# Optimization experiments

Measured on AMD Instinct MI355X. Metric: run time of the kernel, lower is better.

The kernel has to match this reference:

```python
import jax, jax.numpy as jnp
import numpy as np

B, N, C, H, NC, P = 16, 577, 768, 12, 8, 576  # batch, seq(=patches+cls), dim, heads, curves, patches
D = C // H


def setup_inputs() -> dict:
    key = jax.random.key(0)
    ks = jax.random.split(key, 8)
    x = jax.random.normal(ks[0], (B, N, C), jnp.float32)
    qkv_w = jax.random.normal(ks[1], (C, 3 * C), jnp.float32) * 0.02
    proj_w = jax.random.normal(ks[2], (C, C), jnp.float32) * 0.02
    proj_b = jnp.zeros((C,), jnp.float32)
    # learned per-head decay logits; +3 so sigmoid ~0.95 (slow decay, realistic)
    ai_list = jax.random.normal(ks[3], (NC, H), jnp.float32) + 3.0
    mask_weights = jax.random.normal(ks[4], (NC,), jnp.float32) * 0.1 + 1.0 / NC
    normalize = 1.0 + 0.1 * jax.random.normal(ks[5], (H,), jnp.float32)
    # space-filling-curve inverse index permutations (one per curve)
    curve_inds = jnp.stack([
        jax.random.permutation(jax.random.fold_in(ks[6], c), P) for c in range(NC)
    ]).astype(jnp.int32)
    return dict(x=x, qkv_w=qkv_w, proj_w=proj_w, proj_b=proj_b,
                ai_list=ai_list, mask_weights=mask_weights,
                normalize=normalize, curve_inds=curve_inds)


def _build_mask(ai_list, mask_weights, curve_inds):
    # sigmoid(a)^|i-j| gathered by the curve permutation == sigmoid(a)^|ind_i - ind_j|
    a = jax.nn.sigmoid(ai_list)                                  # [NC,H]
    ci = curve_inds.astype(jnp.float32)                          # [NC,P]
    diff = jnp.abs(ci[:, :, None] - ci[:, None, :])              # [NC,P,P]
    Mc = a[:, :, None, None] ** diff[:, None, :, :]              # [NC,H,P,P]
    Mp = jnp.einsum('c,chpq->hpq', mask_weights, Mc)             # weighted sum over curves
    # cls-token row/col: each curve contributes ones -> sum of weights
    sw = jnp.sum(mask_weights)
    M = jnp.pad(Mp, ((0, 0), (1, 0), (1, 0)))                    # [H,N,N]
    M = M.at[:, 0, :].set(sw)
    M = M.at[:, :, 0].set(sw)
    return M


def reference(x, qkv_w, proj_w, proj_b, ai_list, mask_weights, normalize, curve_inds):
    qkv = (x @ qkv_w).reshape(B, N, 3, H, D)
    q = jnp.transpose(qkv[:, :, 0], (0, 2, 1, 3))                # [B,H,N,D]
    k = jnp.transpose(qkv[:, :, 1], (0, 2, 1, 3))
    v = jnp.transpose(qkv[:, :, 2], (0, 2, 1, 3))
    # NOTE: original overwrites self.scale with the bool `scale`=True -> multiply by 1
    attn = jnp.einsum('bhnd,bhmd->bhnm', q, k)                   # [B,H,N,N]
    M = _build_mask(ai_list, mask_weights, curve_inds)           # [H,N,N]
    attn = attn * M[None] * normalize[None, :, None, None]       # method='mul_v1'
    attn = jax.nn.softmax(attn, axis=-1)
    out = jnp.einsum('bhnm,bhmd->bhnd', attn, v)
    out = jnp.transpose(out, (0, 2, 1, 3)).reshape(B, N, C)
    return out @ proj_w + proj_b
```

## Files before the change

kernel.cpp:

```cpp
#include <hip/hip_runtime.h>


typedef _Float16 f16;
typedef _Float16 half8 __attribute__((ext_vector_type(8)));
typedef _Float16 half4 __attribute__((ext_vector_type(4)));
typedef float floatx4 __attribute__((ext_vector_type(4)));

#define DEVINL __device__ __forceinline__

#define Bb 16
#define NN 577
#define CC 768
#define HH 12
#define DD 64
#define MM (Bb * NN)
#define VTLD 584
#define MLD 580
#define CLD 136

DEVINL void async_copy16(void* lds, const void* g) {
  __builtin_amdgcn_global_load_lds(
      (const __attribute__((address_space(1))) void*)g,
      (__attribute__((address_space(3))) void*)lds, 16, 0, 0);
}

DEVINL half8 ld_swz(const f16* lds, int row, int chunk) {
  return *(const half8*)(lds + row * 64 + ((chunk ^ (row & 7)) << 3));
}

DEVINL int xcd_swizzle(int orig, int nwg) {
  int q = nwg >> 3, r = nwg & 7;
  int xcd = orig & 7, loc = orig >> 3;
  return (xcd < r ? xcd * (q + 1) : r * (q + 1) + (xcd - r) * q) + loc;
}

__global__ void cvt_kernel(const float* __restrict__ in, f16* __restrict__ out, int n) {
  int i = (blockIdx.x * blockDim.x + threadIdx.x) * 4;
  if (i >= n) return;
  float4 v = *(const float4*)(in + i);
  half4 o = {(f16)v.x, (f16)v.y, (f16)v.z, (f16)v.w};
  *(half4*)(out + i) = o;
}

__global__ void transpose_cvt(const float* __restrict__ in, f16* __restrict__ out,
                              int N3, int K) {
  __shared__ float t[32][33];
  const int k0 = blockIdx.x * 32, n0 = blockIdx.y * 32;
  const int tx = threadIdx.x & 31, ty = threadIdx.x >> 5;
#pragma unroll
  for (int p = 0; p < 4; ++p)
    t[ty + p * 8][tx] = in[(size_t)(k0 + ty + p * 8) * N3 + n0 + tx];
  __syncthreads();
#pragma unroll
  for (int p = 0; p < 4; ++p)
    out[(size_t)(n0 + ty + p * 8) * K + k0 + tx] = (f16)t[tx][ty + p * 8];
}

__global__ void mask_kernel(const float* __restrict__ ai, const float* __restrict__ mw,
                            const float* __restrict__ nrm, const int* __restrict__ ci,
                            float* __restrict__ Mb) {
  const int i = blockIdx.x;
  const int h = blockIdx.y;
  __shared__ float la_s[8], wv_s[8], cif[8], swn_s;
  int tid = threadIdx.x;
  if (tid < 8) {
    float av = ai[tid * 12 + h];
    float a = 1.f / (1.f + __expf(-av));
    la_s[tid] = __logf(a);
    wv_s[tid] = mw[tid];
    cif[tid] = (i > 0) ? (float)ci[tid * 576 + (i - 1)] : 0.f;
  }
  if (tid == 0) {
    float s = 0.f;
    for (int c = 0; c < 8; ++c) s += mw[c];
    swn_s = s * nrm[h] * 1.44269504088896f;
  }
  __syncthreads();
  const float nr = nrm[h] * 1.44269504088896f;
  float* row = Mb + ((size_t)h * NN + i) * MLD;
  for (int j = tid; j < NN; j += blockDim.x) {
    float val;
    if (i == 0 || j == 0) {
      val = swn_s;
    } else {
      float acc = 0.f;
#pragma unroll
      for (int c = 0; c < 8; ++c) {
        float d = fabsf(cif[c] - (float)ci[c * 576 + (j - 1)]);
        acc += wv_s[c] * __expf(la_s[c] * d);
      }
      val = acc * nr;
    }
    row[j] = val;
  }
}

DEVINL void gemm_mainloop(const f16* __restrict__ A, const f16* __restrict__ Bt,
                          int arow0, int brow0, int maxar,
                          f16* SMEM, floatx4 acc[4][4], int tid) {
  const int lane = tid & 63;
  const int wid = tid >> 6;
  const int wr = wid >> 1, wc = wid & 1;
  const int l15 = lane & 15, g = lane >> 4;
  const int r_ = tid >> 3, cp_ = tid & 7;
  const int lc_ = (cp_ ^ (r_ & 7)) << 3;

  auto stage = [&](f16* As, f16* Bs, int k0) {
#pragma unroll
    for (int q = 0; q < 4; ++q) {
      int idx = q * 256 + tid;
      int r = q * 32 + r_;
      int ar = arow0 + r; if (ar > maxar) ar = maxar;
      async_copy16(As + idx * 8, A + (size_t)ar * CC + k0 + lc_);
      async_copy16(Bs + idx * 8, Bt + (size_t)(brow0 + r) * CC + k0 + lc_);
    }
  };
  auto compute = [&](const f16* As, const f16* Bs) {
#pragma unroll
    for (int kk = 0; kk < 2; ++kk) {
      half8 af[4], bf[4];
#pragma unroll
      for (int mi = 0; mi < 4; ++mi) af[mi] = ld_swz(As, wr * 64 + mi * 16 + l15, kk * 4 + g);
#pragma unroll
      for (int ni = 0; ni < 4; ++ni) bf[ni] = ld_swz(Bs, wc * 64 + ni * 16 + l15, kk * 4 + g);
#pragma unroll
      for (int mi = 0; mi < 4; ++mi)
#pragma unroll
        for (int ni = 0; ni < 4; ++ni)
          acc[mi][ni] = __builtin_amdgcn_mfma_f32_16x16x32_f16(af[mi], bf[ni], acc[mi][ni], 0, 0, 0);
    }
  };

  const int nt = CC / 64;
  stage(SMEM, SMEM + 8192, 0);
#pragma unroll 1
  for (int t = 0; t < nt; ++t) {
    f16* cAs = (t & 1) ? SMEM + 16384 : SMEM;
    f16* cBs = (t & 1) ? SMEM + 24576 : SMEM + 8192;
    f16* nAs = (t & 1) ? SMEM : SMEM + 16384;
    f16* nBs = (t & 1) ? SMEM + 8192 : SMEM + 24576;
    if (t + 1 < nt) {
      stage(nAs, nBs, (t + 1) * 64);
      asm volatile("s_waitcnt vmcnt(8)" ::: "memory");
    } else {
      asm volatile("s_waitcnt vmcnt(0)" ::: "memory");
    }
    __builtin_amdgcn_s_barrier();
    __builtin_amdgcn_sched_barrier(0);
    compute(cAs, cBs);
    __builtin_amdgcn_s_barrier();
  }
}

__global__ __launch_bounds__(256, 2)
void gemm_qkv(const f16* __restrict__ A, const f16* __restrict__ Bt,
              f16* __restrict__ qb, f16* __restrict__ kb, f16* __restrict__ vt) {
  __shared__ __align__(16) f16 SMEM[32768];
  floatx4 acc[4][4] = {};
  const int nwg = 18 * 73;
  const int wgid = xcd_swizzle(blockIdx.y * gridDim.x + blockIdx.x, nwg);
  const int m0 = (wgid / 18) * 128, n0 = (wgid % 18) * 128;
  gemm_mainloop(A, Bt, m0, n0, MM - 1, SMEM, acc, threadIdx.x);
  const int tid = threadIdx.x, lane = tid & 63, wid = tid >> 6;
  const int wr = wid >> 1, wc = wid & 1, l15 = lane & 15, g = lane >> 4;
  const int t = n0 / CC;
  const int h0 = (n0 - t * CC) >> 6;
  if (t < 2) {
#pragma unroll
    for (int mi = 0; mi < 4; ++mi)
#pragma unroll
      for (int ni = 0; ni < 4; ++ni)
#pragma unroll
        for (int r = 0; r < 4; ++r)
          SMEM[(wr * 64 + mi * 16 + 4 * g + r) * CLD + wc * 64 + ni * 16 + l15] =
              (f16)acc[mi][ni][r];
    __syncthreads();
    f16* dst = (t == 0) ? qb : kb;
#pragma unroll
    for (int p = 0; p < 8; ++p) {
      int c = p * 256 + tid;
      int ml = c >> 4, n3c = (c & 15) << 3;
      int mg = m0 + ml;
      if (mg < MM) {
        int b = mg / NN, n = mg - b * NN;
        int h = h0 + (n3c >> 6), d0 = n3c & 63;
        half8 v = *(const half8*)(SMEM + ml * CLD + n3c);
        *(half8*)(dst + ((size_t)(b * HH + h) * NN + n) * DD + d0) = v;
      }
    }
  } else {
#pragma unroll
    for (int mi = 0; mi < 4; ++mi)
#pragma unroll
      for (int ni = 0; ni < 4; ++ni)
#pragma unroll
        for (int r = 0; r < 4; ++r)
          SMEM[(wc * 64 + ni * 16 + l15) * CLD + wr * 64 + mi * 16 + 4 * g + r] =
              (f16)acc[mi][ni][r];
    __syncthreads();
#pragma unroll
    for (int p = 0; p < 8; ++p) {
      int c = p * 256 + tid;
      int n3 = c >> 4, mc = (c & 15) << 3;
      int mg = m0 + mc;
      int h = h0 + (n3 >> 6), d = n3 & 63;
      half8 v = *(const half8*)(SMEM + n3 * CLD + mc);
      int b0 = mg / NN, b7 = (mg + 7) / NN;
      if (mg + 7 < MM && b0 == b7) {
        *(half8*)(vt + ((size_t)(b0 * HH + h) * DD + d) * VTLD + (mg - b0 * NN)) = v;
      } else {
#pragma unroll
        for (int e = 0; e < 8; ++e) {
          int m2 = mg + e;
          if (m2 < MM) {
            int b = m2 / NN;
            vt[((size_t)(b * HH + h) * DD + d) * VTLD + (m2 - b * NN)] = v[e];
          }
        }
      }
    }
  }
}

__global__ __launch_bounds__(256, 2)
void gemm_proj(const f16* __restrict__ A, const f16* __restrict__ Bt,
               const float* __restrict__ bias, float* __restrict__ out) {
  __shared__ __align__(16) f16 SMEM[32768];
  floatx4 acc[4][4] = {};
  const int nwg = 6 * 73;
  const int wgid = xcd_swizzle(blockIdx.y * gridDim.x + blockIdx.x, nwg);
  const int m0 = (wgid / 6) * 128, n0 = (wgid % 6) * 128;
  gemm_mainloop(A, Bt, m0, n0, MM - 1, SMEM, acc, threadIdx.x);
  const int lane = threadIdx.x & 63, wid = threadIdx.x >> 6;
  const int wr = wid >> 1, wc = wid & 1, l15 = lane & 15, g = lane >> 4;
#pragma unroll
  for (int mi = 0; mi < 4; ++mi)
#pragma unroll
    for (int ni = 0; ni < 4; ++ni)
#pragma unroll
      for (int r = 0; r < 4; ++r) {
        int m = m0 + wr * 64 + mi * 16 + 4 * g + r;
        if (m >= MM) continue;
        int n = n0 + wc * 64 + ni * 16 + l15;
        out[(size_t)m * CC + n] = acc[mi][ni][r] + bias[n];
      }
}

__global__ __launch_bounds__(512, 4)
void attn_kernel(const f16* __restrict__ qb, const f16* __restrict__ kb,
                 const f16* __restrict__ vt, const float* __restrict__ Mb,
                 f16* __restrict__ aout) {
  __shared__ f16 Ks[2][64 * 64];
  __shared__ f16 Vs[2][64 * 64];
  const int D0 = (blockIdx.z * gridDim.y + blockIdx.y) * gridDim.x + blockIdx.x;
  const int wgid = xcd_swizzle(D0, 5 * HH * Bb);
  const int it = wgid % 5;
  const int rem = wgid / 5;
  const int b = rem % Bb, h = rem / Bb;
  const int tid = threadIdx.x, lane = tid & 63, wid = tid >> 6;
  const int l15 = lane & 15, g = lane >> 4;
  const size_t bh = (size_t)b * HH + h;
  const f16* qbh = qb + bh * NN * DD;
  const f16* kbh = kb + bh * NN * DD;
  const f16* vbh = vt + bh * DD * VTLD;
  const float* Mh = Mb + (size_t)h * NN * MLD;
  const int row0w = it * 128 + wid * 16;

  half8 qB0, qB1;
  {
    int qr = row0w + l15; if (qr > NN - 1) qr = NN - 1;
    const f16* qp = qbh + (size_t)qr * DD + g * 8;
    qB0 = *(const half8*)qp;
    qB1 = *(const half8*)(qp + 32);
  }
  const float* Mrow;
  {
    int r0 = row0w + l15; if (r0 > NN - 1) r0 = NN - 1;
    Mrow = Mh + (size_t)r0 * MLD + 4 * g;
  }

  floatx4 acc[4] = {};
  float lsum = 0.f;
  float mrun = -3e38f;

  const int sr_ = tid >> 3, scp_ = tid & 7;
  const int slc_ = (scp_ ^ (sr_ & 7)) << 3;
  auto stage = [&](f16* Kd, f16* Vd, int j0) {
    int j = j0 + sr_; if (j > NN - 1) j = NN - 1;
    async_copy16(Kd + tid * 8, kbh + (size_t)j * DD + slc_);
    async_copy16(Vd + tid * 8, vbh + (size_t)sr_ * VTLD + j0 + slc_);
  };
  auto ldmask = [&](floatx4 m4[4], int j0) {
#pragma unroll
    for (int jt = 0; jt < 4; ++jt)
      m4[jt] = *(const floatx4*)(Mrow + j0 + jt * 16);
  };
  auto compute = [&](const f16* Kc, const f16* Vc, floatx4 m4[4], int j0) {
    floatx4 sf[4];
#pragma unroll
    for (int jt = 0; jt < 4; ++jt) {
      half8 ka0 = ld_swz(Kc, jt * 16 + l15, g);
      half8 ka1 = ld_swz(Kc, jt * 16 + l15, 4 + g);
      floatx4 z = {0.f, 0.f, 0.f, 0.f};
      z = __builtin_amdgcn_mfma_f32_16x16x32_f16(ka0, qB0, z, 0, 0, 0);
      z = __builtin_amdgcn_mfma_f32_16x16x32_f16(ka1, qB1, z, 0, 0, 0);
      sf[jt] = z;
    }
#pragma unroll
    for (int jt = 0; jt < 4; ++jt)
#pragma unroll
      for (int r = 0; r < 4; ++r) sf[jt][r] *= m4[jt][r];
    if (j0 + 64 > NN) {
#pragma unroll
      for (int jt = 0; jt < 4; ++jt)
#pragma unroll
        for (int r = 0; r < 4; ++r)
          if (j0 + jt * 16 + 4 * g + r >= NN) sf[jt][r] = -3e38f;
    }
    float pj[4];
#pragma unroll
    for (int jt = 0; jt < 4; ++jt)
      pj[jt] = fmaxf(fmaxf(sf[jt][0], sf[jt][1]), fmaxf(sf[jt][2], sf[jt][3]));
    float pmax = fmaxf(fmaxf(pj[0], pj[1]), fmaxf(pj[2], pj[3]));
    pmax = fmaxf(pmax, __shfl_xor(pmax, 16));
    pmax = fmaxf(pmax, __shfl_xor(pmax, 32));
    if (!__all(pmax - mrun <= 8.f)) {
      float mnew = fmaxf(mrun, pmax);
      float fac = __builtin_amdgcn_exp2f(mrun - mnew);
      mrun = mnew;
      lsum *= fac;
#pragma unroll
      for (int dt = 0; dt < 4; ++dt)
#pragma unroll
        for (int r = 0; r < 4; ++r) acc[dt][r] *= fac;
    }
    half4 pB[4];
    float lsj[4];
#pragma unroll
    for (int jt = 0; jt < 4; ++jt) {
      half4 pb;
      float p0 = __builtin_amdgcn_exp2f(sf[jt][0] - mrun);
      float p1 = __builtin_amdgcn_exp2f(sf[jt][1] - mrun);
      float p2 = __builtin_amdgcn_exp2f(sf[jt][2] - mrun);
      float p3 = __builtin_amdgcn_exp2f(sf[jt][3] - mrun);
      pb[0] = (f16)p0; pb[1] = (f16)p1; pb[2] = (f16)p2; pb[3] = (f16)p3;
      lsj[jt] = (p0 + p1) + (p2 + p3);
      pB[jt] = pb;
    }
    lsum += (lsj[0] + lsj[1]) + (lsj[2] + lsj[3]);
#pragma unroll
    for (int dt = 0; dt < 4; ++dt)
#pragma unroll
      for (int jt = 0; jt < 4; ++jt) {
        int c16 = (jt * 2 + (g >> 1)) ^ (l15 & 7);
        half4 va = *(const half4*)(Vc + (dt * 16 + l15) * 64 + (c16 << 3) + (g & 1) * 4);
        acc[dt] = __builtin_amdgcn_mfma_f32_16x16x16f16(va, pB[jt], acc[dt], 0, 0, 0);
      }
  };

  floatx4 m4A[4], m4B[4];
  stage(Ks[0], Vs[0], 0);
  ldmask(m4A, 0);

#pragma unroll 1
  for (int t = 0; t < 10; t += 2) {
    ldmask(m4B, (t + 1) * 64);
    asm volatile("s_waitcnt vmcnt(4)" ::: "memory");
    __builtin_amdgcn_s_barrier();
    __builtin_amdgcn_sched_barrier(0);
    stage(Ks[1], Vs[1], (t + 1) * 64);
    compute(Ks[0], Vs[0], m4A, t * 64);
    const int j2 = (t + 2 < 10) ? (t + 2) * 64 : 0;
    ldmask(m4A, j2);
    asm volatile("s_waitcnt vmcnt(4)" ::: "memory");
    __builtin_amdgcn_s_barrier();
    __builtin_amdgcn_sched_barrier(0);
    stage(Ks[0], Vs[0], j2);
    compute(Ks[1], Vs[1], m4B, (t + 1) * 64);
  }

  {
    float v = lsum;
    v += __shfl_xor(v, 16);
    v += __shfl_xor(v, 32);
    float linv = 1.f / v;
    int n = row0w + l15;
    if (n < NN) {
#pragma unroll
      for (int dt = 0; dt < 4; ++dt) {
        half4 o;
#pragma unroll
        for (int r = 0; r < 4; ++r) o[r] = (f16)(acc[dt][r] * linv);
        *(half4*)(aout + ((size_t)(b * NN + n)) * CC + h * DD + dt * 16 + 4 * g) = o;
      }
    }
  }
}

extern "C" void kernel_launch(void* const* d_in, const int* in_sizes, int n_in,
                              void* d_out, int out_size, void* d_ws, size_t ws_size,
                              hipStream_t stream) {
  const float* x    = (const float*)d_in[0];
  const float* qkvw = (const float*)d_in[1];
  const float* pw   = (const float*)d_in[2];
  const float* pb   = (const float*)d_in[3];
  const float* ai   = (const float*)d_in[4];
  const float* mw   = (const float*)d_in[5];
  const float* nrm  = (const float*)d_in[6];
  const int*   ci   = (const int*)d_in[7];
  float* out = (float*)d_out;

  char* wsb = (char*)d_ws;
  size_t off = 0;
  auto alloc = [&](size_t bytes) {
    char* p = wsb + off;
    off += (bytes + 255) & ~(size_t)255;
    return p;
  };
  f16*   x_h  = (f16*)alloc((size_t)MM * CC * 2);
  f16*   w_t  = (f16*)alloc((size_t)3 * CC * CC * 2);
  f16*   pw_t = (f16*)alloc((size_t)CC * CC * 2);
  float* Mb   = (float*)alloc((size_t)HH * NN * MLD * 4 + 1024);
  f16*   qb   = (f16*)alloc((size_t)Bb * HH * NN * DD * 2);
  f16*   kb   = (f16*)alloc((size_t)Bb * HH * NN * DD * 2);
  f16*   vt   = (f16*)alloc((size_t)Bb * HH * DD * VTLD * 2);
  (void)alloc(4096);
  f16* aout = x_h;

  cvt_kernel<<<(MM * CC / 4 + 255) / 256, 256, 0, stream>>>(x, x_h, MM * CC);
  transpose_cvt<<<dim3(CC / 32, 3 * CC / 32), 256, 0, stream>>>(qkvw, w_t, 3 * CC, CC);
  transpose_cvt<<<dim3(CC / 32, CC / 32), 256, 0, stream>>>(pw, pw_t, CC, CC);
  mask_kernel<<<dim3(NN, HH), 256, 0, stream>>>(ai, mw, nrm, ci, Mb);
  gemm_qkv<<<dim3(18, 73), 256, 0, stream>>>(x_h, w_t, qb, kb, vt);
  attn_kernel<<<dim3(5, HH, Bb), 512, 0, stream>>>(qb, kb, vt, Mb, aout);
  gemm_proj<<<dim3(6, 73), 256, 0, stream>>>(aout, pw_t, pb, out);
}
```

Measured before the change: 159.4 us.

## Merge prep kernels into one launch and use 256x128 GEMM tiles with 512 threads

Folds the fp16 convert, the two weight transpose-converts and the mask build into a single prep kernel that dispatches on block index, removing three kernel launches. Both GEMMs move from 128x128 tiles with 256 threads to 256x128 tiles with 512 threads, so each staged B tile is reused by twice as many A rows. LDS grows to 96KB per block, which limits occupancy. The larger M tile also raises tail waste, since the 9232 rows now fill 37 row tiles instead of 73.

Measured after the change: 150.3 us. -5.7%, faster.

```diff
diff --git a/kernel.cpp b/kernel.cpp
--- a/kernel.cpp
+++ b/kernel.cpp
@@ -17,6 +17,7 @@
 #define VTLD 584
 #define MLD 580
 #define CLD 136
+#define TLD 264
 
 DEVINL void async_copy16(void* lds, const void* g) {
   __builtin_amdgcn_global_load_lds(
@@ -34,64 +35,71 @@
   return (xcd < r ? xcd * (q + 1) : r * (q + 1) + (xcd - r) * q) + loc;
 }
 
-__global__ void cvt_kernel(const float* __restrict__ in, f16* __restrict__ out, int n) {
-  int i = (blockIdx.x * blockDim.x + threadIdx.x) * 4;
-  if (i >= n) return;
-  float4 v = *(const float4*)(in + i);
-  half4 o = {(f16)v.x, (f16)v.y, (f16)v.z, (f16)v.w};
-  *(half4*)(out + i) = o;
-}
-
-__global__ void transpose_cvt(const float* __restrict__ in, f16* __restrict__ out,
-                              int N3, int K) {
-  __shared__ float t[32][33];
-  const int k0 = blockIdx.x * 32, n0 = blockIdx.y * 32;
-  const int tx = threadIdx.x & 31, ty = threadIdx.x >> 5;
-#pragma unroll
-  for (int p = 0; p < 4; ++p)
-    t[ty + p * 8][tx] = in[(size_t)(k0 + ty + p * 8) * N3 + n0 + tx];
-  __syncthreads();
-#pragma unroll
-  for (int p = 0; p < 4; ++p)
-    out[(size_t)(n0 + ty + p * 8) * K + k0 + tx] = (f16)t[tx][ty + p * 8];
-}
-
-__global__ void mask_kernel(const float* __restrict__ ai, const float* __restrict__ mw,
-                            const float* __restrict__ nrm, const int* __restrict__ ci,
-                            float* __restrict__ Mb) {
-  const int i = blockIdx.x;
-  const int h = blockIdx.y;
-  __shared__ float la_s[8], wv_s[8], cif[8], swn_s;
-  int tid = threadIdx.x;
-  if (tid < 8) {
-    float av = ai[tid * 12 + h];
-    float a = 1.f / (1.f + __expf(-av));
-    la_s[tid] = __logf(a);
-    wv_s[tid] = mw[tid];
-    cif[tid] = (i > 0) ? (float)ci[tid * 576 + (i - 1)] : 0.f;
-  }
-  if (tid == 0) {
-    float s = 0.f;
-    for (int c = 0; c < 8; ++c) s += mw[c];
-    swn_s = s * nrm[h] * 1.44269504088896f;
-  }
-  __syncthreads();
-  const float nr = nrm[h] * 1.44269504088896f;
-  float* row = Mb + ((size_t)h * NN + i) * MLD;
-  for (int j = tid; j < NN; j += blockDim.x) {
-    float val;
-    if (i == 0 || j == 0) {
-      val = swn_s;
-    } else {
-      float acc = 0.f;
-#pragma unroll
-      for (int c = 0; c < 8; ++c) {
-        float d = fabsf(cif[c] - (float)ci[c * 576 + (j - 1)]);
-        acc += wv_s[c] * __expf(la_s[c] * d);
-      }
-      val = acc * nr;
-    }
-    row[j] = val;
+__global__ __launch_bounds__(256)
+void prep_kernel(const float* __restrict__ x, const float* __restrict__ qkvw,
+                 const float* __restrict__ pw, const float* __restrict__ ai,
+                 const float* __restrict__ mw, const float* __restrict__ nrm,
+                 const int* __restrict__ ci, f16* __restrict__ x_h,
+                 f16* __restrict__ w_t, f16* __restrict__ pw_t,
+                 float* __restrict__ Mb) {
+  __shared__ float shm[32 * 33];
+  const int bid = blockIdx.x;
+  const int tid = threadIdx.x;
+  if (bid < 6924) {
+    int i = (bid * 256 + tid) * 4;
+    float4 v = *(const float4*)(x + i);
+    half4 o = {(f16)v.x, (f16)v.y, (f16)v.z, (f16)v.w};
+    *(half4*)(x_h + i) = o;
+  } else if (bid < 9228) {
+    bool isq = bid < 8652;
+    int b2 = bid - (isq ? 6924 : 8652);
+    int N3 = isq ? 3 * CC : CC;
+    const float* in = isq ? qkvw : pw;
+    f16* out = isq ? w_t : pw_t;
+    const int k0 = (b2 % 24) * 32, n0 = (b2 / 24) * 32;
+    const int tx = tid & 31, ty = tid >> 5;
+#pragma unroll
+    for (int p = 0; p < 4; ++p)
+      shm[(ty + p * 8) * 33 + tx] = in[(size_t)(k0 + ty + p * 8) * N3 + n0 + tx];
+    __syncthreads();
+#pragma unroll
+    for (int p = 0; p < 4; ++p)
+      out[(size_t)(n0 + ty + p * 8) * CC + k0 + tx] = (f16)shm[tx * 33 + ty + p * 8];
+  } else {
+    int b4 = bid - 9228;
+    int i = b4 % NN, h = b4 / NN;
+    float* la_s = shm; float* wv_s = shm + 8; float* cif = shm + 16;
+    float* swn_s = shm + 24;
+    if (tid < 8) {
+      float av = ai[tid * 12 + h];
+      float a = 1.f / (1.f + __expf(-av));
+      la_s[tid] = __logf(a);
+      wv_s[tid] = mw[tid];
+      cif[tid] = (i > 0) ? (float)ci[tid * 576 + (i - 1)] : 0.f;
+    }
+    if (tid == 0) {
+      float s = 0.f;
+      for (int c = 0; c < 8; ++c) s += mw[c];
+      swn_s[0] = s * nrm[h] * 1.44269504088896f;
+    }
+    __syncthreads();
+    const float nr = nrm[h] * 1.44269504088896f;
+    float* row = Mb + ((size_t)h * NN + i) * MLD;
+    for (int j = tid; j < NN; j += 256) {
+      float val;
+      if (i == 0 || j == 0) {
+        val = swn_s[0];
+      } else {
+        float acc = 0.f;
+#pragma unroll
+        for (int c = 0; c < 8; ++c) {
+          float d = fabsf(cif[c] - (float)ci[c * 576 + (j - 1)]);
+          acc += wv_s[c] * __expf(la_s[c] * d);
+        }
+        val = acc * nr;
+      }
+      row[j] = val;
+    }
   }
 }
 
@@ -108,11 +116,14 @@
   auto stage = [&](f16* As, f16* Bs, int k0) {
 #pragma unroll
     for (int q = 0; q < 4; ++q) {
-      int idx = q * 256 + tid;
-      int r = q * 32 + r_;
+      int r = q * 64 + r_;
       int ar = arow0 + r; if (ar > maxar) ar = maxar;
-      async_copy16(As + idx * 8, A + (size_t)ar * CC + k0 + lc_);
-      async_copy16(Bs + idx * 8, Bt + (size_t)(brow0 + r) * CC + k0 + lc_);
+      async_copy16(As + (q * 512 + tid) * 8, A + (size_t)ar * CC + k0 + lc_);
+    }
+#pragma unroll
+    for (int q = 0; q < 2; ++q) {
+      int r = q * 64 + r_;
+      async_copy16(Bs + (q * 512 + tid) * 8, Bt + (size_t)(brow0 + r) * CC + k0 + lc_);
     }
   };
   auto compute = [&](const f16* As, const f16* Bs) {
@@ -132,16 +143,16 @@
   };
 
   const int nt = CC / 64;
-  stage(SMEM, SMEM + 8192, 0);
+  stage(SMEM, SMEM + 16384, 0);
 #pragma unroll 1
   for (int t = 0; t < nt; ++t) {
-    f16* cAs = (t & 1) ? SMEM + 16384 : SMEM;
-    f16* cBs = (t & 1) ? SMEM + 24576 : SMEM + 8192;
-    f16* nAs = (t & 1) ? SMEM : SMEM + 16384;
-    f16* nBs = (t & 1) ? SMEM + 8192 : SMEM + 24576;
+    f16* cAs = (t & 1) ? SMEM + 24576 : SMEM;
+    f16* cBs = (t & 1) ? SMEM + 40960 : SMEM + 16384;
+    f16* nAs = (t & 1) ? SMEM : SMEM + 24576;
+    f16* nBs = (t & 1) ? SMEM + 16384 : SMEM + 40960;
     if (t + 1 < nt) {
       stage(nAs, nBs, (t + 1) * 64);
-      asm volatile("s_waitcnt vmcnt(8)" ::: "memory");
+      asm volatile("s_waitcnt vmcnt(6)" ::: "memory");
     } else {
       asm volatile("s_waitcnt vmcnt(0)" ::: "memory");
     }
@@ -152,14 +163,14 @@
   }
 }
 
-__global__ __launch_bounds__(256, 2)
+__global__ __launch_bounds__(512, 2)
 void gemm_qkv(const f16* __restrict__ A, const f16* __restrict__ Bt,
               f16* __restrict__ qb, f16* __restrict__ kb, f16* __restrict__ vt) {
-  __shared__ __align__(16) f16 SMEM[32768];
+  __shared__ __align__(16) f16 SMEM[49152];
   floatx4 acc[4][4] = {};
-  const int nwg = 18 * 73;
+  const int nwg = 18 * 37;
   const int wgid = xcd_swizzle(blockIdx.y * gridDim.x + blockIdx.x, nwg);
-  const int m0 = (wgid / 18) * 128, n0 = (wgid % 18) * 128;
+  const int m0 = (wgid / 18) * 256, n0 = (wgid % 18) * 128;
   gemm_mainloop(A, Bt, m0, n0, MM - 1, SMEM, acc, threadIdx.x);
   const int tid = threadIdx.x, lane = tid & 63, wid = tid >> 6;
   const int wr = wid >> 1, wc = wid & 1, l15 = lane & 15, g = lane >> 4;
@@ -178,7 +189,7 @@
     f16* dst = (t == 0) ? qb : kb;
 #pragma unroll
     for (int p = 0; p < 8; ++p) {
-      int c = p * 256 + tid;
+      int c = p * 512 + tid;
       int ml = c >> 4, n3c = (c & 15) << 3;
       int mg = m0 + ml;
       if (mg < MM) {
@@ -195,18 +206,18 @@
       for (int ni = 0; ni < 4; ++ni)
 #pragma unroll
         for (int r = 0; r < 4; ++r)
-          SMEM[(wc * 64 + ni * 16 + l15) * CLD + wr * 64 + mi * 16 + 4 * g + r] =
+          SMEM[(wc * 64 + ni * 16 + l15) * TLD + wr * 64 + mi * 16 + 4 * g + r] =
               (f16)acc[mi][ni][r];
     __syncthreads();
 #pragma unroll
     for (int p = 0; p < 8; ++p) {
-      int c = p * 256 + tid;
-      int n3 = c >> 4, mc = (c & 15) << 3;
+      int c = p * 512 + tid;
+      int n3 = c >> 5, mc = (c & 31) << 3;
       int mg = m0 + mc;
       int h = h0 + (n3 >> 6), d = n3 & 63;
-      half8 v = *(const half8*)(SMEM + n3 * CLD + mc);
-      int b0 = mg / NN, b7 = (mg + 7) / NN;
-      if (mg + 7 < MM && b0 == b7) {
+      half8 v = *(const half8*)(SMEM + n3 * TLD + mc);
+      int b0 = mg / NN;
+      if (mg + 7 < MM && (mg + 7) / NN == b0) {
         *(half8*)(vt + ((size_t)(b0 * HH + h) * DD + d) * VTLD + (mg - b0 * NN)) = v;
       } else {
 #pragma unroll
@@ -222,14 +233,14 @@
   }
 }
 
-__global__ __launch_bounds__(256, 2)
+__global__ __launch_bounds__(512, 2)
 void gemm_proj(const f16* __restrict__ A, const f16* __restrict__ Bt,
                const float* __restrict__ bias, float* __restrict__ out) {
-  __shared__ __align__(16) f16 SMEM[32768];
+  __shared__ __align__(16) f16 SMEM[49152];
   floatx4 acc[4][4] = {};
-  const int nwg = 6 * 73;
+  const int nwg = 6 * 37;
   const int wgid = xcd_swizzle(blockIdx.y * gridDim.x + blockIdx.x, nwg);
-  const int m0 = (wgid / 6) * 128, n0 = (wgid % 6) * 128;
+  const int m0 = (wgid / 6) * 256, n0 = (wgid % 6) * 128;
   gemm_mainloop(A, Bt, m0, n0, MM - 1, SMEM, acc, threadIdx.x);
   const int lane = threadIdx.x & 63, wid = threadIdx.x >> 6;
   const int wr = wid >> 1, wc = wid & 1, l15 = lane & 15, g = lane >> 4;
@@ -427,11 +438,9 @@
   (void)alloc(4096);
   f16* aout = x_h;
 
-  cvt_kernel<<<(MM * CC / 4 + 255) / 256, 256, 0, stream>>>(x, x_h, MM * CC);
-  transpose_cvt<<<dim3(CC / 32, 3 * CC / 32), 256, 0, stream>>>(qkvw, w_t, 3 * CC, CC);
-  transpose_cvt<<<dim3(CC / 32, CC / 32), 256, 0, stream>>>(pw, pw_t, CC, CC);
-  mask_kernel<<<dim3(NN, HH), 256, 0, stream>>>(ai, mw, nrm, ci, Mb);
-  gemm_qkv<<<dim3(18, 73), 256, 0, stream>>>(x_h, w_t, qb, kb, vt);
+  prep_kernel<<<16152, 256, 0, stream>>>(x, qkvw, pw, ai, mw, nrm, ci,
+                                         x_h, w_t, pw_t, Mb);
+  gemm_qkv<<<dim3(18, 37), 512, 0, stream>>>(x_h, w_t, qb, kb, vt);
   attn_kernel<<<dim3(5, HH, Bb), 512, 0, stream>>>(qb, kb, vt, Mb, aout);
-  gemm_proj<<<dim3(6, 73), 256, 0, stream>>>(aout, pw_t, pb, out);
-}
+  gemm_proj<<<dim3(6, 37), 512, 0, stream>>>(aout, pw_t, pb, out);
+}
```
